# Kernel tuning notes

Hardware: AMD Instinct MI355X
Metric: run time of the kernel (lower is better)

The kernel has to match this reference:

```python
import jax, jax.numpy as jnp
import numpy as np

NUM_FREQS = 8
TEMPERATURE = 100.0
DOWNSAMPLE = 64
GRID = 8
D_OUT = 512


def fourier_embed(x):
    # x: [M, 2] -> [M, NUM_FREQS*2*2], order: per freq [sin(f*x), cos(f*x)]
    freqs = TEMPERATURE ** (jnp.arange(NUM_FREQS, dtype=jnp.float32) / NUM_FREQS)
    xf = x[:, None, :] * freqs[None, :, None]  # [M, F, 2]
    feats = jnp.stack([jnp.sin(xf), jnp.cos(xf)], axis=2)  # [M, F, 2, 2]
    return feats.reshape(x.shape[0], -1)  # [M, 32]


def mlp(x, W1, b1, W2, b2, W3, b3):
    h = jax.nn.silu(x @ W1 + b1)
    h = jax.nn.silu(h @ W2 + b2)
    return h @ W3 + b3


def scatter_to_grid(drags, emb):
    # drags: [BV, N, 2] (pixel coords), emb: [BV, N, 512]
    BV, N, _ = drags.shape
    r = drags[..., 0].astype(jnp.int32) // DOWNSAMPLE  # [BV, N]
    c = drags[..., 1].astype(jnp.int32) // DOWNSAMPLE
    idx = r * GRID + c  # flat cell index in [0, 64)
    b_idx = jnp.arange(BV)[:, None]
    grid = jnp.zeros((BV, GRID * GRID, D_OUT), emb.dtype).at[b_idx, idx].add(emb)
    # -> [BV, 512, 8, 8]
    return grid.transpose(0, 2, 1).reshape(BV, D_OUT, GRID, GRID)


def setup_inputs() -> dict:
    key = jax.random.key(0)
    ks = jax.random.split(key, 8)
    B, V, N = 8, 8, 1024
    IMG = GRID * DOWNSAMPLE  # 512
    drags_start = jax.random.uniform(ks[0], (B, V, N, 2), jnp.float32) * IMG
    drags_end = jax.random.uniform(ks[1], (B, V, N, 2), jnp.float32) * IMG
    pd = NUM_FREQS * 2 * 2  # 32
    W1 = jax.random.normal(ks[2], (pd, 128), jnp.float32) * (1.0 / np.sqrt(pd))
    b1 = jnp.zeros((128,), jnp.float32)
    W2 = jax.random.normal(ks[3], (128, 256), jnp.float32) * (1.0 / np.sqrt(128))
    b2 = jnp.zeros((256,), jnp.float32)
    W3 = jax.random.normal(ks[4], (256, 512), jnp.float32) * (1.0 / np.sqrt(256))
    b3 = jnp.zeros((512,), jnp.float32)
    return dict(drags_start=drags_start, drags_end=drags_end,
                W1=W1, b1=b1, W2=W2, b2=b2, W3=W3, b3=b3)


def reference(drags_start, drags_end, W1, b1, W2, b2, W3, b3):
    B, V, N, _ = drags_start.shape
    BV = B * V
    ds = drags_start.reshape(BV, N, 2)
    de = drags_end.reshape(BV, N, 2)

    def embed(d):  # [BV, N, 2] -> [BV, N, 512]
        feats = fourier_embed(d.reshape(BV * N, 2))  # no_grad in torch
        return mlp(feats, W1, b1, W2, b2, W3, b3).reshape(BV, N, D_OUT)

    emb_s = embed(ds)
    emb_e = embed(de)
    merge_s = scatter_to_grid(ds, emb_s)
    merge_e = scatter_to_grid(de, emb_e)
    return jnp.concatenate([merge_s, merge_e], axis=1)  # [BV, 1024, 8, 8]
```

## Files before the change

kernel.cpp:

```cpp
#include <hip/hip_runtime.h>
#include <hip/hip_bf16.h>

typedef _Float16 half8 __attribute__((ext_vector_type(8)));
typedef _Float16 half4v __attribute__((ext_vector_type(4)));
typedef float floatx4 __attribute__((ext_vector_type(4)));
typedef unsigned int uint4v __attribute__((ext_vector_type(4)));

__device__ const float FREQS[8] = {
    1.0f, 1.7782794100389228f, 3.1622776601683795f, 5.623413251903491f,
    10.0f, 17.78279410038923f, 31.622776601683793f, 56.23413251903491f};

__device__ inline void fsincos(float m, float& s, float& c) {
  constexpr double I2PI_D = 0.15915494309189533576888376337251;
  constexpr float HI = (float)I2PI_D;
  constexpr float LO = (float)(I2PI_D - (double)HI);
  float k = rintf(m * HI);
  float f = fmaf(m, HI, -k);
  f = fmaf(m, LO, f);
  s = __builtin_amdgcn_sinf(f);
  c = __builtin_amdgcn_cosf(f);
}

__device__ inline float fsilu(float x) {
  return x * __builtin_amdgcn_rcpf(1.f + __expf(-x));
}

__global__ __launch_bounds__(256) void prep_weights(
    const float* __restrict__ W1, const float* __restrict__ W2,
    const float* __restrict__ W3, _Float16* __restrict__ W1t,
    _Float16* __restrict__ W2t, _Float16* __restrict__ W3f) {
  int tid = blockIdx.x * blockDim.x + threadIdx.x;
  int stride = gridDim.x * blockDim.x;
  for (int i = tid; i < 128 * 32; i += stride) {
    int n = i >> 5, k = i & 31;
    W1t[i] = (_Float16)W1[k * 128 + n];
  }
  for (int i = tid; i < 256 * 128; i += stride) {
    int n = i >> 7, k = i & 127;
    W2t[i] = (_Float16)W2[k * 256 + n];
  }
  for (int i = tid; i < 512 * 256; i += stride) {
    int k = i >> 9, n = i & 511;
    int it = n >> 4, ln = n & 15, ks = k >> 5, q = (k >> 3) & 3, j = k & 7;
    W3f[((size_t)(it * 8 + ks) * 64 + q * 16 + ln) * 8 + j] = (_Float16)W3[i];
  }
}

__global__ __launch_bounds__(512, 4) void embed_scatter(
    const float* __restrict__ dstart, const float* __restrict__ dend,
    const float* __restrict__ b1, const float* __restrict__ b2,
    const _Float16* __restrict__ W1t, const _Float16* __restrict__ W2t,
    _Float16* __restrict__ swz, int* __restrict__ counts) {
  __shared__ _Float16 h1f[16384];
  __shared__ _Float16 W1lds[4096];
  __shared__ _Float16 ohs[8192];
  __shared__ float b1lds[128];
  __shared__ unsigned char cellb[256];
  __shared__ int hist[64];

  int bid = blockIdx.x;
  int bv = bid >> 3, tsel = (bid >> 2) & 1, pg = bid & 3;
  const float* src = tsel ? dend : dstart;
  int tid = threadIdx.x;
  int lane = tid & 63, w = tid >> 6, ln = lane & 15, q = lane >> 4;

  *(half8*)&W1lds[tid * 8] = *(const half8*)&W1t[tid * 8];
  if (tid < 128) b1lds[tid] = b1[tid];
  if (tid < 64) hist[tid] = 0;
  __syncthreads();

  int pbase = bv * 1024 + pg * 256;
  if (tid < 256) {
    float2 xy = *(const float2*)&src[(size_t)(pbase + tid) * 2];
    int cell = ((int)xy.x >> 6) * 8 + ((int)xy.y >> 6);
    cellb[tid] = (unsigned char)cell;
    atomicAdd(&hist[cell], 1);
  }

  half8 w2f[2][4];
  float b2v[2];
  for (int nt = 0; nt < 2; nt++) {
    int n = w * 32 + nt * 16 + ln;
    b2v[nt] = b2[n];
    for (int ks = 0; ks < 4; ks++)
      w2f[nt][ks] = *(const half8*)&W2t[n * 128 + ks * 32 + q * 8];
  }
  floatx4 sacc[4][2];
  for (int mc = 0; mc < 4; mc++)
    for (int nt = 0; nt < 2; nt++) sacc[mc][nt] = (floatx4){0.f, 0.f, 0.f, 0.f};

  float fA = FREQS[2 * q], fB = FREQS[2 * q + 1];
  __syncthreads();

  for (int c = 0; c < 2; c++) {
    for (int e = 0; e < 2; e++) {
      int eid = tid * 2 + e;
      int l2 = eid & 63, mc = (eid >> 6) & 3, tt = eid >> 8;
      unsigned m = (unsigned)(mc * 16 + (l2 & 15));
      int pb = c * 128 + tt * 32 + (l2 >> 4) * 4;
      unsigned ca = *(const unsigned*)&cellb[pb];
      unsigned cb = *(const unsigned*)&cellb[pb + 16];
      unsigned d0 = ((ca & 255) == m ? 0x3C00u : 0u) | (((ca >> 8) & 255) == m ? 0x3C000000u : 0u);
      unsigned d1 = (((ca >> 16) & 255) == m ? 0x3C00u : 0u) | ((ca >> 24) == m ? 0x3C000000u : 0u);
      unsigned d2 = ((cb & 255) == m ? 0x3C00u : 0u) | (((cb >> 8) & 255) == m ? 0x3C000000u : 0u);
      unsigned d3 = (((cb >> 16) & 255) == m ? 0x3C00u : 0u) | ((cb >> 24) == m ? 0x3C000000u : 0u);
      uint4v u = {d0, d1, d2, d3};
      *(half8*)&ohs[eid * 8] = __builtin_bit_cast(half8, u);
    }
    int pl = c * 128 + w * 16 + ln;
    float2 xy = *(const float2*)&src[(size_t)(pbase + pl) * 2];
    half8 fb;
    {
      float s, cc2;
      fsincos(xy.x * fA, s, cc2); fb[0] = (_Float16)s; fb[2] = (_Float16)cc2;
      fsincos(xy.y * fA, s, cc2); fb[1] = (_Float16)s; fb[3] = (_Float16)cc2;
      fsincos(xy.x * fB, s, cc2); fb[4] = (_Float16)s; fb[6] = (_Float16)cc2;
      fsincos(xy.y * fB, s, cc2); fb[5] = (_Float16)s; fb[7] = (_Float16)cc2;
    }
    for (int mtW = 0; mtW < 8; mtW++) {
      half8 w1f = *(const half8*)&W1lds[(mtW * 16 + ln) * 32 + q * 8];
      floatx4 c1 = *(const floatx4*)&b1lds[mtW * 16 + q * 4];
      c1 = __builtin_amdgcn_mfma_f32_16x16x32_f16(w1f, fb, c1, 0, 0, 0);
      half4v hv;
      for (int r = 0; r < 4; r++) hv[r] = (_Float16)fsilu(c1[r]);
      int addr = (((w * 4 + (mtW >> 1)) * 4 + ((mtW & 1) * 2 + (q >> 1))) * 16 + ln) * 8 + (q & 1) * 4;
      *(half4v*)&h1f[addr] = hv;
    }
    __syncthreads();
    for (int t = 0; t < 4; t++) {
      half8 af0[4], af1[4];
      for (int ks = 0; ks < 4; ks++) {
        af0[ks] = *(const half8*)&h1f[((((2 * t) * 4 + ks) * 4 + q) * 16 + ln) * 8];
        af1[ks] = *(const half8*)&h1f[((((2 * t + 1) * 4 + ks) * 4 + q) * 16 + ln) * 8];
      }
      half8 oh[4];
      for (int mc = 0; mc < 4; mc++)
        oh[mc] = *(const half8*)&ohs[((t * 4 + mc) * 64 + lane) * 8];
      for (int nt = 0; nt < 2; nt++) {
        floatx4 c0 = {b2v[nt], b2v[nt], b2v[nt], b2v[nt]};
        floatx4 c1 = c0;
        for (int ks = 0; ks < 4; ks++) {
          c0 = __builtin_amdgcn_mfma_f32_16x16x32_f16(af0[ks], w2f[nt][ks], c0, 0, 0, 0);
          c1 = __builtin_amdgcn_mfma_f32_16x16x32_f16(af1[ks], w2f[nt][ks], c1, 0, 0, 0);
        }
        half8 hb;
        for (int r = 0; r < 4; r++) {
          hb[r] = (_Float16)fsilu(c0[r]);
          hb[4 + r] = (_Float16)fsilu(c1[r]);
        }
        for (int mc = 0; mc < 4; mc++)
          sacc[mc][nt] = __builtin_amdgcn_mfma_f32_16x16x32_f16(oh[mc], hb, sacc[mc][nt], 0, 0, 0);
      }
    }
    __syncthreads();
  }
  for (int mc = 0; mc < 4; mc++)
    for (int nt = 0; nt < 2; nt++) {
      half4v hv;
      for (int r = 0; r < 4; r++) hv[r] = (_Float16)sacc[mc][nt][r];
      *(half4v*)&swz[((((size_t)bid * 4 + mc) * 16 + w * 2 + nt) * 64 + lane) * 4] = hv;
    }
  if (tid < 64) counts[bid * 64 + tid] = hist[tid];
}

__global__ __launch_bounds__(256) void layer3(
    const _Float16* __restrict__ swz, const int* __restrict__ counts,
    const _Float16* __restrict__ W3f, const float* __restrict__ b3,
    float* __restrict__ out) {
  __shared__ _Float16 bfrag[16384];
  __shared__ float cnt_s[64];
  int bvts = blockIdx.x;
  int ch2 = blockIdx.y;
  int tid = threadIdx.x;
  for (int it = 0; it < 16; it++) {
    int idx = it * 256 + tid;
    int mc = idx >> 10, wnt = (idx >> 6) & 15, l = idx & 63;
    int qq = l >> 4, lnn = l & 15;
    size_t base = (size_t)bvts * 16384 + (size_t)idx;
    half4v s = (*(const half4v*)&swz[base * 4] +
                *(const half4v*)&swz[(base + 4096) * 4]) +
               (*(const half4v*)&swz[(base + 8192) * 4] +
                *(const half4v*)&swz[(base + 12288) * 4]);
    int abase = ((mc * 8 + (wnt >> 1)) * 4 + ((wnt & 1) * 2 + (lnn >> 3))) * 16;
    for (int r = 0; r < 4; r++)
      bfrag[(abase + qq * 4 + r) * 8 + (lnn & 7)] = s[r];
  }
  if (tid < 64) {
    int base = bvts * 256 + tid;
    cnt_s[tid] = (float)(counts[base] + counts[base + 64] +
                         counts[base + 128] + counts[base + 192]);
  }
  __syncthreads();
  int lane = tid & 63, w = tid >> 6, ln = lane & 15, q = lane >> 4;
  floatx4 acc[2][4];
  for (int i2 = 0; i2 < 2; i2++)
    for (int cn = 0; cn < 4; cn++) acc[i2][cn] = (floatx4){0.f, 0.f, 0.f, 0.f};
  for (int ks = 0; ks < 8; ks++) {
    half8 bf[4];
    for (int cn = 0; cn < 4; cn++)
      bf[cn] = *(const half8*)&bfrag[(((cn * 8 + ks) * 4 + q) * 16 + ln) * 8];
    for (int i2 = 0; i2 < 2; i2++) {
      int I = ch2 * 8 + w * 2 + i2;
      half8 wf = *(const half8*)&W3f[(size_t)((I * 8 + ks) * 64 + lane) * 8];
      for (int cn = 0; cn < 4; cn++)
        acc[i2][cn] = __builtin_amdgcn_mfma_f32_16x16x32_f16(wf, bf[cn], acc[i2][cn], 0, 0, 0);
    }
  }
  for (int i2 = 0; i2 < 2; i2++) {
    int nb = ch2 * 128 + (w * 2 + i2) * 16;
    floatx4 b3v = *(const floatx4*)&b3[nb + q * 4];
    for (int cn = 0; cn < 4; cn++) {
      float cf = cnt_s[cn * 16 + ln];
      for (int r = 0; r < 4; r++)
        out[((size_t)bvts * 512 + nb + q * 4 + r) * 64 + cn * 16 + ln] =
            acc[i2][cn][r] + cf * b3v[r];
    }
  }
}

extern "C" void kernel_launch(void* const* d_in, const int* in_sizes, int n_in,
                              void* d_out, int out_size, void* d_ws, size_t ws_size,
                              hipStream_t stream) {
  const float* dstart = (const float*)d_in[0];
  const float* dend = (const float*)d_in[1];
  const float* W1 = (const float*)d_in[2];
  const float* b1 = (const float*)d_in[3];
  const float* W2 = (const float*)d_in[4];
  const float* b2 = (const float*)d_in[5];
  const float* W3 = (const float*)d_in[6];
  const float* b3 = (const float*)d_in[7];
  float* out = (float*)d_out;

  char* ws = (char*)d_ws;
  _Float16* W1t = (_Float16*)(ws);
  _Float16* W2t = (_Float16*)(ws + 8192);
  _Float16* W3f = (_Float16*)(ws + 73728);
  _Float16* swz = (_Float16*)(ws + 335872);
  int* counts = (int*)(ws + 335872 + 16777216);

  hipLaunchKernelGGL(prep_weights, dim3(64), dim3(256), 0, stream,
                     W1, W2, W3, W1t, W2t, W3f);
  hipLaunchKernelGGL(embed_scatter, dim3(512), dim3(512), 0, stream,
                     dstart, dend, b1, b2, W1t, W2t, swz, counts);
  hipLaunchKernelGGL(layer3, dim3(128, 4), dim3(256), 0, stream,
                     swz, counts, W3f, b3, out);
}
```

Before: 128.4 us.

## Fuse W1/W2 prep into embed kernel and build one-hot scatter fragments in registers

Drops the W1/W2 transpose-and-convert from the prep kernel: embed_scatter now reads fp32 W1 and W2 directly and converts them while loading, and prep_w3 writes one half8 per thread. The one-hot scatter matrix is built in registers per 16-point tile and fed to 16x16x16 MFMAs, removing the ohs LDS buffer and its stores and loads. Layer-2 output is transposed through LDS so it is written to the workspace already in layer3's fragment layout, which turns layer3's reduction into contiguous half8 loads and stores. The cost is strided uncoalesced global reads of W1 and W2 in every one of the 512 blocks, and more MFMA instructions for the scatter step.

```diff
diff --git a/kernel.cpp b/kernel.cpp
--- a/kernel.cpp
+++ b/kernel.cpp
@@ -4,7 +4,7 @@
 typedef _Float16 half8 __attribute__((ext_vector_type(8)));
 typedef _Float16 half4v __attribute__((ext_vector_type(4)));
 typedef float floatx4 __attribute__((ext_vector_type(4)));
-typedef unsigned int uint4v __attribute__((ext_vector_type(4)));
+typedef unsigned int uint2v __attribute__((ext_vector_type(2)));
 
 __device__ const float FREQS[8] = {
     1.0f, 1.7782794100389228f, 3.1622776601683795f, 5.623413251903491f,
@@ -25,35 +25,25 @@
   return x * __builtin_amdgcn_rcpf(1.f + __expf(-x));
 }
 
-__global__ __launch_bounds__(256) void prep_weights(
-    const float* __restrict__ W1, const float* __restrict__ W2,
-    const float* __restrict__ W3, _Float16* __restrict__ W1t,
-    _Float16* __restrict__ W2t, _Float16* __restrict__ W3f) {
-  int tid = blockIdx.x * blockDim.x + threadIdx.x;
-  int stride = gridDim.x * blockDim.x;
-  for (int i = tid; i < 128 * 32; i += stride) {
-    int n = i >> 5, k = i & 31;
-    W1t[i] = (_Float16)W1[k * 128 + n];
-  }
-  for (int i = tid; i < 256 * 128; i += stride) {
-    int n = i >> 7, k = i & 127;
-    W2t[i] = (_Float16)W2[k * 256 + n];
-  }
-  for (int i = tid; i < 512 * 256; i += stride) {
-    int k = i >> 9, n = i & 511;
-    int it = n >> 4, ln = n & 15, ks = k >> 5, q = (k >> 3) & 3, j = k & 7;
-    W3f[((size_t)(it * 8 + ks) * 64 + q * 16 + ln) * 8 + j] = (_Float16)W3[i];
-  }
+__global__ __launch_bounds__(256) void prep_w3(const float* __restrict__ W3,
+                                               _Float16* __restrict__ W3f) {
+  int t = blockIdx.x * 256 + threadIdx.x;
+  int ln = t & 15, q = (t >> 4) & 3, ks = (t >> 6) & 7, I = t >> 9;
+  half8 v;
+  for (int j = 0; j < 8; j++)
+    v[j] = (_Float16)W3[(size_t)(ks * 32 + q * 8 + j) * 512 + I * 16 + ln];
+  *(half8*)&W3f[(size_t)t * 8] = v;
 }
 
 __global__ __launch_bounds__(512, 4) void embed_scatter(
     const float* __restrict__ dstart, const float* __restrict__ dend,
-    const float* __restrict__ b1, const float* __restrict__ b2,
-    const _Float16* __restrict__ W1t, const _Float16* __restrict__ W2t,
+    const float* __restrict__ W1, const float* __restrict__ b1,
+    const float* __restrict__ W2, const float* __restrict__ b2,
     _Float16* __restrict__ swz, int* __restrict__ counts) {
-  __shared__ _Float16 h1f[16384];
-  __shared__ _Float16 W1lds[4096];
-  __shared__ _Float16 ohs[8192];
+  __shared__ _Float16 smem[16384 + 4096];
+  _Float16* h1f = smem;
+  _Float16* W1lds = smem + 16384;
+  _Float16* h2t = smem;
   __shared__ float b1lds[128];
   __shared__ unsigned char cellb[256];
   __shared__ int hist[64];
@@ -64,7 +54,12 @@
   int tid = threadIdx.x;
   int lane = tid & 63, w = tid >> 6, ln = lane & 15, q = lane >> 4;
 
-  *(half8*)&W1lds[tid * 8] = *(const half8*)&W1t[tid * 8];
+  {
+    int n = tid >> 2, kb = (tid & 3) * 8;
+    half8 v;
+    for (int j = 0; j < 8; j++) v[j] = (_Float16)W1[(kb + j) * 128 + n];
+    *(half8*)&W1lds[n * 32 + kb] = v;
+  }
   if (tid < 128) b1lds[tid] = b1[tid];
   if (tid < 64) hist[tid] = 0;
   __syncthreads();
@@ -82,8 +77,12 @@
   for (int nt = 0; nt < 2; nt++) {
     int n = w * 32 + nt * 16 + ln;
     b2v[nt] = b2[n];
-    for (int ks = 0; ks < 4; ks++)
-      w2f[nt][ks] = *(const half8*)&W2t[n * 128 + ks * 32 + q * 8];
+    for (int ks = 0; ks < 4; ks++) {
+      half8 v;
+      for (int j = 0; j < 8; j++)
+        v[j] = (_Float16)W2[(ks * 32 + q * 8 + j) * 256 + n];
+      w2f[nt][ks] = v;
+    }
   }
   floatx4 sacc[4][2];
   for (int mc = 0; mc < 4; mc++)
@@ -93,20 +92,6 @@
   __syncthreads();
 
   for (int c = 0; c < 2; c++) {
-    for (int e = 0; e < 2; e++) {
-      int eid = tid * 2 + e;
-      int l2 = eid & 63, mc = (eid >> 6) & 3, tt = eid >> 8;
-      unsigned m = (unsigned)(mc * 16 + (l2 & 15));
-      int pb = c * 128 + tt * 32 + (l2 >> 4) * 4;
-      unsigned ca = *(const unsigned*)&cellb[pb];
-      unsigned cb = *(const unsigned*)&cellb[pb + 16];
-      unsigned d0 = ((ca & 255) == m ? 0x3C00u : 0u) | (((ca >> 8) & 255) == m ? 0x3C000000u : 0u);
-      unsigned d1 = (((ca >> 16) & 255) == m ? 0x3C00u : 0u) | ((ca >> 24) == m ? 0x3C000000u : 0u);
-      unsigned d2 = ((cb & 255) == m ? 0x3C00u : 0u) | (((cb >> 8) & 255) == m ? 0x3C000000u : 0u);
-      unsigned d3 = (((cb >> 16) & 255) == m ? 0x3C00u : 0u) | ((cb >> 24) == m ? 0x3C000000u : 0u);
-      uint4v u = {d0, d1, d2, d3};
-      *(half8*)&ohs[eid * 8] = __builtin_bit_cast(half8, u);
-    }
     int pl = c * 128 + w * 16 + ln;
     float2 xy = *(const float2*)&src[(size_t)(pbase + pl) * 2];
     half8 fb;
@@ -127,39 +112,45 @@
       *(half4v*)&h1f[addr] = hv;
     }
     __syncthreads();
-    for (int t = 0; t < 4; t++) {
-      half8 af0[4], af1[4];
-      for (int ks = 0; ks < 4; ks++) {
-        af0[ks] = *(const half8*)&h1f[((((2 * t) * 4 + ks) * 4 + q) * 16 + ln) * 8];
-        af1[ks] = *(const half8*)&h1f[((((2 * t + 1) * 4 + ks) * 4 + q) * 16 + ln) * 8];
+    for (int tt = 0; tt < 8; tt++) {
+      half8 af[4];
+      for (int ks = 0; ks < 4; ks++)
+        af[ks] = *(const half8*)&h1f[(((tt * 4 + ks) * 4 + q) * 16 + ln) * 8];
+      unsigned ca = *(const unsigned*)&cellb[c * 128 + tt * 16 + q * 4];
+      unsigned e0 = ca & 255, e1 = (ca >> 8) & 255, e2 = (ca >> 16) & 255, e3 = ca >> 24;
+      half4v oh[4];
+      for (int mc = 0; mc < 4; mc++) {
+        unsigned m = (unsigned)(mc * 16 + ln);
+        unsigned d0 = (e0 == m ? 0x3C00u : 0u) | (e1 == m ? 0x3C000000u : 0u);
+        unsigned d1 = (e2 == m ? 0x3C00u : 0u) | (e3 == m ? 0x3C000000u : 0u);
+        uint2v u = {d0, d1};
+        oh[mc] = __builtin_bit_cast(half4v, u);
       }
-      half8 oh[4];
-      for (int mc = 0; mc < 4; mc++)
-        oh[mc] = *(const half8*)&ohs[((t * 4 + mc) * 64 + lane) * 8];
       for (int nt = 0; nt < 2; nt++) {
-        floatx4 c0 = {b2v[nt], b2v[nt], b2v[nt], b2v[nt]};
-        floatx4 c1 = c0;
-        for (int ks = 0; ks < 4; ks++) {
-          c0 = __builtin_amdgcn_mfma_f32_16x16x32_f16(af0[ks], w2f[nt][ks], c0, 0, 0, 0);
-          c1 = __builtin_amdgcn_mfma_f32_16x16x32_f16(af1[ks], w2f[nt][ks], c1, 0, 0, 0);
-        }
-        half8 hb;
-        for (int r = 0; r < 4; r++) {
-          hb[r] = (_Float16)fsilu(c0[r]);
-          hb[4 + r] = (_Float16)fsilu(c1[r]);
-        }
+        floatx4 cc = {b2v[nt], b2v[nt], b2v[nt], b2v[nt]};
+        for (int ks = 0; ks < 4; ks++)
+          cc = __builtin_amdgcn_mfma_f32_16x16x32_f16(af[ks], w2f[nt][ks], cc, 0, 0, 0);
+        half4v hb;
+        for (int r = 0; r < 4; r++) hb[r] = (_Float16)fsilu(cc[r]);
         for (int mc = 0; mc < 4; mc++)
-          sacc[mc][nt] = __builtin_amdgcn_mfma_f32_16x16x32_f16(oh[mc], hb, sacc[mc][nt], 0, 0, 0);
+          sacc[mc][nt] = __builtin_amdgcn_mfma_f32_16x16x16f16(oh[mc], hb, sacc[mc][nt], 0, 0, 0);
       }
     }
     __syncthreads();
   }
+
   for (int mc = 0; mc < 4; mc++)
-    for (int nt = 0; nt < 2; nt++) {
-      half4v hv;
-      for (int r = 0; r < 4; r++) hv[r] = (_Float16)sacc[mc][nt][r];
-      *(half4v*)&swz[((((size_t)bid * 4 + mc) * 16 + w * 2 + nt) * 64 + lane) * 4] = hv;
-    }
+    for (int nt = 0; nt < 2; nt++)
+      for (int r = 0; r < 4; r++)
+        h2t[(mc * 16 + q * 4 + r) * 264 + w * 32 + nt * 16 + ln] =
+            (_Float16)sacc[mc][nt][r];
+  __syncthreads();
+  for (int i = 0; i < 4; i++) {
+    int g = i * 512 + tid;
+    int lnn = g & 15, qq = (g >> 4) & 3, ks2 = (g >> 6) & 7, cn = g >> 9;
+    half8 v = *(const half8*)&h2t[(cn * 16 + lnn) * 264 + ks2 * 32 + qq * 8];
+    *(half8*)&swz[(size_t)bid * 16384 + (size_t)g * 8] = v;
+  }
   if (tid < 64) counts[bid * 64 + tid] = hist[tid];
 }
 
@@ -167,23 +158,19 @@
     const _Float16* __restrict__ swz, const int* __restrict__ counts,
     const _Float16* __restrict__ W3f, const float* __restrict__ b3,
     float* __restrict__ out) {
-  __shared__ _Float16 bfrag[16384];
+  __shared__ _Float16 blds[16384];
   __shared__ float cnt_s[64];
   int bvts = blockIdx.x;
   int ch2 = blockIdx.y;
   int tid = threadIdx.x;
-  for (int it = 0; it < 16; it++) {
-    int idx = it * 256 + tid;
-    int mc = idx >> 10, wnt = (idx >> 6) & 15, l = idx & 63;
-    int qq = l >> 4, lnn = l & 15;
-    size_t base = (size_t)bvts * 16384 + (size_t)idx;
-    half4v s = (*(const half4v*)&swz[base * 4] +
-                *(const half4v*)&swz[(base + 4096) * 4]) +
-               (*(const half4v*)&swz[(base + 8192) * 4] +
-                *(const half4v*)&swz[(base + 12288) * 4]);
-    int abase = ((mc * 8 + (wnt >> 1)) * 4 + ((wnt & 1) * 2 + (lnn >> 3))) * 16;
-    for (int r = 0; r < 4; r++)
-      bfrag[(abase + qq * 4 + r) * 8 + (lnn & 7)] = s[r];
+  const _Float16* sb = swz + (size_t)bvts * 65536;
+  for (int i = 0; i < 8; i++) {
+    int g = i * 256 + tid;
+    half8 v0 = *(const half8*)&sb[(size_t)g * 8];
+    half8 v1 = *(const half8*)&sb[16384 + (size_t)g * 8];
+    half8 v2 = *(const half8*)&sb[32768 + (size_t)g * 8];
+    half8 v3 = *(const half8*)&sb[49152 + (size_t)g * 8];
+    *(half8*)&blds[g * 8] = (v0 + v1) + (v2 + v3);
   }
   if (tid < 64) {
     int base = bvts * 256 + tid;
@@ -198,7 +185,7 @@
   for (int ks = 0; ks < 8; ks++) {
     half8 bf[4];
     for (int cn = 0; cn < 4; cn++)
-      bf[cn] = *(const half8*)&bfrag[(((cn * 8 + ks) * 4 + q) * 16 + ln) * 8];
+      bf[cn] = *(const half8*)&blds[(((cn * 8 + ks) * 4 + q) * 16 + ln) * 8];
     for (int i2 = 0; i2 < 2; i2++) {
       int I = ch2 * 8 + w * 2 + i2;
       half8 wf = *(const half8*)&W3f[(size_t)((I * 8 + ks) * 64 + lane) * 8];
@@ -232,16 +219,13 @@
   float* out = (float*)d_out;
 
   char* ws = (char*)d_ws;
-  _Float16* W1t = (_Float16*)(ws);
-  _Float16* W2t = (_Float16*)(ws + 8192);
-  _Float16* W3f = (_Float16*)(ws + 73728);
-  _Float16* swz = (_Float16*)(ws + 335872);
-  int* counts = (int*)(ws + 335872 + 16777216);
-
-  hipLaunchKernelGGL(prep_weights, dim3(64), dim3(256), 0, stream,
-                     W1, W2, W3, W1t, W2t, W3f);
+  _Float16* W3f = (_Float16*)(ws);
+  _Float16* swz = (_Float16*)(ws + 262144);
+  int* counts = (int*)(ws + 262144 + 16777216);
+
+  hipLaunchKernelGGL(prep_w3, dim3(64), dim3(256), 0, stream, W3, W3f);
   hipLaunchKernelGGL(embed_scatter, dim3(512), dim3(512), 0, stream,
-                     dstart, dend, b1, b2, W1t, W2t, swz, counts);
+                     dstart, dend, W1, b1, W2, b2, swz, counts);
   hipLaunchKernelGGL(layer3, dim3(128, 4), dim3(256), 0, stream,
                      swz, counts, W3f, b3, out);
 }
```

New measurement: 120.1 us. 6.5% less time.
